# Kernel optimization log

Hardware: AMD Instinct MI355X
Metric: run time of the kernel (lower is better)

## Reference

```python
import jax, jax.numpy as jnp
import numpy as np

NUM_AGES = 100
FEAT_DIM = 512
BATCH = 4096
TEMPERATURE = 0.1
EPS = 1e-6


def setup_inputs() -> dict:
    key = jax.random.key(0)
    k1, k2, k3 = jax.random.split(key, 3)
    z_age = jax.random.normal(k1, (BATCH, FEAT_DIM), dtype=jnp.float32)
    ages = jax.random.randint(k2, (BATCH,), 0, NUM_AGES, dtype=jnp.int64)
    proxies = jax.random.normal(k3, (NUM_AGES, FEAT_DIM), dtype=jnp.float32)
    return {"z_age": z_age, "ages": ages, "proxies": proxies}


def _unit_diff(a, b):
    d = a - b
    return d / (jnp.linalg.norm(d, axis=-1, keepdims=True) + EPS)


def reference(z_age, ages, proxies):
    # Vectorized equivalent of the O(B^2) python double loop.
    # Only pairs with age_i < age_j contribute (age_i > age_j branch is a no-op `...`).
    B = z_age.shape[0]
    A = proxies.shape[0]
    aj = ages.astype(jnp.int32)
    c_cur = proxies[aj]                                   # [B, D]
    c_next = proxies[jnp.minimum(aj + 1, A - 1)]          # [B, D]
    c_prev = proxies[jnp.maximum(aj - 1, 0)]              # [B, D]
    vf = _unit_diff(c_next, c_cur)                        # forward direction per sample j
    vb = _unit_diff(c_prev, c_cur)                        # backward direction per sample j

    # Pairwise norms via Gram matrix: ||z_i - z_j||.
    G = z_age @ z_age.T                                   # [B, B]
    sq = jnp.diagonal(G)                                  # [B]
    d2 = jnp.maximum(sq[:, None] + sq[None, :] - 2.0 * G, 0.0)
    norm = jnp.sqrt(d2)                                   # [B, B]
    denom = norm + EPS

    # dot(v_d_ij, v_f_j) = (z_i . vf_j - z_j . vf_j) / (||z_i - z_j|| + eps)
    Gf = z_age @ vf.T                                     # [B, B], Gf[i, j] = z_i . vf_j
    Gb = z_age @ vb.T
    dot_f = (Gf - jnp.diagonal(Gf)[None, :]) / denom
    dot_b = (Gb - jnp.diagonal(Gb)[None, :]) / denom

    # -log(exp(df/T) / (exp(df/T) + exp(db/T))) = softplus((db - df)/T)
    per_pair = jax.nn.softplus((dot_b - dot_f) / TEMPERATURE)  # [B, B]
    mask = ages[:, None] < ages[None, :]
    loss = jnp.sum(jnp.where(mask, per_pair, 0.0))
    return loss / (B * (B - 1))
```

## Files before the change

kernel.cpp:

```cpp
#include <hip/hip_runtime.h>
#include <hip/hip_bf16.h>

#define NUM_AGES 100
#define FEAT 512
#define BATCH 4096
#define EPSF 1e-6f
#define INV_T 10.0f
#define INV_NORM (1.0f / ((float)BATCH * (float)(BATCH - 1)))

#define BM 128
#define BN 64
#define BK 64
#define NTILES 1056
#define NXCD 8
#define CHUNK (NTILES / NXCD)

typedef __bf16 bf16_t;
typedef __bf16 v8bf __attribute__((ext_vector_type(8)));
typedef float v4f __attribute__((ext_vector_type(4)));

__device__ __forceinline__ void async16(const void* g, void* l) {
  __builtin_amdgcn_global_load_lds(
      (const __attribute__((address_space(1))) void*)g,
      (__attribute__((address_space(3))) void*)l, 16, 0, 0);
}

__global__ __launch_bounds__(256) void prep_kernel(
    const float* __restrict__ z, const int* __restrict__ ages,
    const float* __restrict__ proxies,
    bf16_t* __restrict__ zb, bf16_t* __restrict__ wb,
    float* __restrict__ sq, float* __restrict__ hd,
    int* __restrict__ ages_s, float* __restrict__ out)
{
  int j = blockIdx.x;
  int t = threadIdx.x;
  if (j == 0 && t == 0) out[0] = 0.0f;

  int araw = ages[j];
  int a = araw < 0 ? 0 : (araw > NUM_AGES - 1 ? NUM_AGES - 1 : araw);
  const float* cc = proxies + (size_t)a * FEAT;
  const float* cn = proxies + (size_t)(a + 1 > NUM_AGES - 1 ? NUM_AGES - 1 : a + 1) * FEAT;
  const float* cp = proxies + (size_t)(a - 1 < 0 ? 0 : a - 1) * FEAT;
  const float* zr = z + (size_t)j * FEAT;

  int cnt = 0;
#pragma unroll
  for (int e = 0; e < BATCH / 256; ++e) {
    int k = t + e * 256;
    int ak = ages[k];
    cnt += (ak < araw || (ak == araw && k < j)) ? 1 : 0;
  }

  int c0 = 2 * t;
  float2 cc2 = *(const float2*)(cc + c0);
  float2 cn2 = *(const float2*)(cn + c0);
  float2 cp2 = *(const float2*)(cp + c0);
  float2 z2  = *(const float2*)(zr + c0);
  float df0 = cn2.x - cc2.x, df1 = cn2.y - cc2.y;
  float db0 = cp2.x - cc2.x, db1 = cp2.y - cc2.y;
  float s_ff = df0 * df0 + df1 * df1;
  float s_bb = db0 * db0 + db1 * db1;
  float s_zz = z2.x * z2.x + z2.y * z2.y;
  float s_zf = z2.x * df0 + z2.y * df1;
  float s_zb = z2.x * db0 + z2.y * db1;

  float fcnt = (float)cnt;
#pragma unroll
  for (int off = 32; off > 0; off >>= 1) {
    s_ff += __shfl_down(s_ff, off, 64);
    s_bb += __shfl_down(s_bb, off, 64);
    s_zz += __shfl_down(s_zz, off, 64);
    s_zf += __shfl_down(s_zf, off, 64);
    s_zb += __shfl_down(s_zb, off, 64);
    fcnt += __shfl_down(fcnt, off, 64);
  }
  __shared__ float red[4][6];
  int wv = t >> 6, lane = t & 63;
  if (lane == 0) {
    red[wv][0] = s_ff; red[wv][1] = s_bb; red[wv][2] = s_zz;
    red[wv][3] = s_zf; red[wv][4] = s_zb; red[wv][5] = fcnt;
  }
  __syncthreads();
  float ff = red[0][0] + red[1][0] + red[2][0] + red[3][0];
  float bb = red[0][1] + red[1][1] + red[2][1] + red[3][1];
  float zz = red[0][2] + red[1][2] + red[2][2] + red[3][2];
  float zdf = red[0][3] + red[1][3] + red[2][3] + red[3][3];
  float zdb = red[0][4] + red[1][4] + red[2][4] + red[3][4];
  int rank = (int)(red[0][5] + red[1][5] + red[2][5] + red[3][5]);

  float rf = 1.0f / (sqrtf(ff) + EPSF);
  float rb = 1.0f / (sqrtf(bb) + EPSF);
  int key = rank & 7;
  int c2s = (c0 & ~63) | (((((c0 >> 3) & 7) ^ key) << 3)) | (c0 & 7);
  float w0 = db0 * rb - df0 * rf;
  float w1 = db1 * rb - df1 * rf;
  union { bf16_t h[2]; unsigned u; } uz, uw;
  uz.h[0] = (bf16_t)z2.x; uz.h[1] = (bf16_t)z2.y;
  uw.h[0] = (bf16_t)w0;   uw.h[1] = (bf16_t)w1;
  *(unsigned*)((char*)zb + ((size_t)rank * FEAT + c2s) * 2) = uz.u;
  *(unsigned*)((char*)wb + ((size_t)rank * FEAT + c2s) * 2) = uw.u;
  if (t == 0) {
    sq[rank] = zz;
    hd[rank] = rb * zdb - rf * zdf;
    ages_s[rank] = araw;
  }
}

__global__ __launch_bounds__(256, 2) void pair_kernel(
    const bf16_t* __restrict__ zb, const bf16_t* __restrict__ wb,
    const float* __restrict__ sq, const float* __restrict__ hd,
    const int* __restrict__ ages, float* __restrict__ out)
{
  __shared__ __attribute__((aligned(16))) char lds[2][32768];
  __shared__ float s_sqi[BM];
  __shared__ int   s_agei[BM];
  __shared__ float s_sqj[BN];
  __shared__ float s_hdj[BN];
  __shared__ int   s_agej[BN];
  __shared__ float wsum[4];

  int t = threadIdx.x;
  int wv = t >> 6, lane = t & 63;

  int by = 0, bx = 0;
  {
    int rem = (blockIdx.x & 7) * CHUNK + (blockIdx.x >> 3);
    int done = 0;
    for (int sy = 0; sy < 4 && !done; ++sy) {
      for (int sx = 0; sx < 8 && !done; ++sx) {
        int cnt = 0;
        for (int r = 0; r < 8; ++r) {
          int b = 8 * sy + r;
          int lo = 2 * b; if (lo < 8 * sx) lo = 8 * sx;
          int ww = 8 * sx + 8 - lo; if (ww < 0) ww = 0;
          cnt += ww;
        }
        if (rem < cnt) {
          for (int r = 0; r < 8 && !done; ++r) {
            int b = 8 * sy + r;
            int lo = 2 * b; if (lo < 8 * sx) lo = 8 * sx;
            int ww = 8 * sx + 8 - lo; if (ww < 0) ww = 0;
            if (rem < ww) { by = b; bx = lo + rem; done = 1; }
            else rem -= ww;
          }
        } else {
          rem -= cnt;
        }
      }
    }
  }
  int i0 = by * BM, j0 = bx * BN;

  if (t < BM) {
    s_sqi[t] = sq[i0 + t];
    s_agei[t] = ages[i0 + t];
  } else if (t < BM + BN) {
    int u = t - BM;
    s_sqj[u] = sq[j0 + u];
    s_hdj[u] = hd[j0 + u];
    s_agej[u] = ages[j0 + u];
  }

  v4f accG[4][2], accH[4][2];
#pragma unroll
  for (int a = 0; a < 4; ++a)
#pragma unroll
    for (int b = 0; b < 2; ++b) {
      accG[a][b] = (v4f){0.f, 0.f, 0.f, 0.f};
      accH[a][b] = (v4f){0.f, 0.f, 0.f, 0.f};
    }

  int wm = wv >> 1, wn = wv & 1;
  int lm = lane & 15, q = lane >> 4;
  int psw0 = ((q     ) ^ (lm & 7)) * 16;
  int psw1 = ((q + 4 ) ^ (lm & 7)) * 16;

  int loff = (lane >> 3) * FEAT + (lane & 7) * 8;
  const bf16_t* baseA = zb + (size_t)i0 * FEAT + loff;
  const bf16_t* baseZ = zb + (size_t)j0 * FEAT + loff;
  const bf16_t* baseW = wb + (size_t)j0 * FEAT + loff;

#pragma unroll
  for (int c = 0; c < 4; ++c) {
    int chunk = wv * 4 + c;
    async16(baseA + (size_t)chunk * 8 * FEAT, lds[0] + chunk * 1024);
  }
#pragma unroll
  for (int c = 0; c < 2; ++c) {
    int chunk = wv * 2 + c;
    async16(baseZ + (size_t)chunk * 8 * FEAT, lds[0] + 16384 + chunk * 1024);
    async16(baseW + (size_t)chunk * 8 * FEAT, lds[0] + 24576 + chunk * 1024);
  }
  __syncthreads();

  int cur = 0;
  for (int it = 0; it < FEAT / BK; ++it) {
    if (it + 1 < FEAT / BK) {
      int k0n = (it + 1) * BK;
      char* nb = lds[cur ^ 1];
#pragma unroll
      for (int c = 0; c < 4; ++c) {
        int chunk = wv * 4 + c;
        async16(baseA + (size_t)chunk * 8 * FEAT + k0n, nb + chunk * 1024);
      }
#pragma unroll
      for (int c = 0; c < 2; ++c) {
        int chunk = wv * 2 + c;
        async16(baseZ + (size_t)chunk * 8 * FEAT + k0n, nb + 16384 + chunk * 1024);
        async16(baseW + (size_t)chunk * 8 * FEAT + k0n, nb + 24576 + chunk * 1024);
      }
    }

    const char* cb = lds[cur];
#pragma unroll
    for (int s = 0; s < 2; ++s) {
      int psw = s ? psw1 : psw0;
      v8bf afr[4], bz[2], bw[2];
#pragma unroll
      for (int mi = 0; mi < 4; ++mi) {
        int r = wm * 64 + mi * 16 + lm;
        afr[mi] = *(const v8bf*)(cb + r * 128 + psw);
      }
#pragma unroll
      for (int ni = 0; ni < 2; ++ni) {
        int r = wn * 32 + ni * 16 + lm;
        bz[ni] = *(const v8bf*)(cb + 16384 + r * 128 + psw);
        bw[ni] = *(const v8bf*)(cb + 24576 + r * 128 + psw);
      }
#pragma unroll
      for (int mi = 0; mi < 4; ++mi)
#pragma unroll
        for (int ni = 0; ni < 2; ++ni) {
          accG[mi][ni] = __builtin_amdgcn_mfma_f32_16x16x32_bf16(afr[mi], bz[ni], accG[mi][ni], 0, 0, 0);
          accH[mi][ni] = __builtin_amdgcn_mfma_f32_16x16x32_bf16(afr[mi], bw[ni], accH[mi][ni], 0, 0, 0);
        }
    }

    if (it + 1 < FEAT / BK) {
      __syncthreads();
      cur ^= 1;
    }
  }

  float tsum = 0.f;
#pragma unroll
  for (int ni = 0; ni < 2; ++ni) {
    int jl = wn * 32 + ni * 16 + lm;
    float sqj = s_sqj[jl];
    float hdj = s_hdj[jl];
    int aj = s_agej[jl];
#pragma unroll
    for (int mi = 0; mi < 4; ++mi) {
#pragma unroll
      for (int r = 0; r < 4; ++r) {
        int il = wm * 64 + mi * 16 + q * 4 + r;
        float g = accG[mi][ni][r];
        float h = accH[mi][ni][r];
        float d2 = fmaxf(s_sqi[il] + sqj - 2.0f * g, 1e-12f);
        float rs = __builtin_amdgcn_rsqf(d2);
        float arg = (h - hdj) * INV_T * rs;
        float sp = fmaxf(arg, 0.0f) + __logf(1.0f + __expf(-fabsf(arg)));
        tsum += (s_agei[il] < aj) ? sp : 0.0f;
      }
    }
  }

#pragma unroll
  for (int off = 32; off > 0; off >>= 1) tsum += __shfl_down(tsum, off, 64);
  if (lane == 0) wsum[wv] = tsum;
  __syncthreads();
  if (t == 0)
    atomicAdd(out, (wsum[0] + wsum[1] + wsum[2] + wsum[3]) * INV_NORM);
}

extern "C" void kernel_launch(void* const* d_in, const int* in_sizes, int n_in,
                              void* d_out, int out_size, void* d_ws, size_t ws_size,
                              hipStream_t stream) {
  const float* z = (const float*)d_in[0];
  const int* ages = (const int*)d_in[1];
  const float* proxies = (const float*)d_in[2];
  float* out = (float*)d_out;

  char* ws = (char*)d_ws;
  bf16_t* zb = (bf16_t*)ws;
  bf16_t* wb = (bf16_t*)(ws + (size_t)4 * 1024 * 1024);
  size_t o = (size_t)8 * 1024 * 1024;
  float* sq      = (float*)(ws + o);
  float* hd      = (float*)(ws + o + 16384);
  int*   ages_s  = (int*)  (ws + o + 32768);

  prep_kernel<<<BATCH, 256, 0, stream>>>(z, ages, proxies, zb, wb, sq, hd, ages_s, out);
  pair_kernel<<<NTILES, 256, 0, stream>>>(zb, wb, sq, hd, ages_s, out);
}
```

Before: 112.1 us.

## Prefetch two K-stages ahead with fine-grained vmcnt waits and MFMA priority

Restructures the double-buffered K loop so two stages are in flight at once. The next-next stage is issued after a barrier, and only the current stage's loads are waited on with an explicit vmcnt(8) rather than a full __syncthreads drain. MFMA blocks are wrapped in s_setprio to favour matrix issue, and sched_barriers pin the instruction order. The aim is to hide global-to-LDS latency behind compute, at the cost of hand-maintained waitcnt counts that become fragile if the number of loads per stage changes.

```diff
diff --git a/kernel.cpp b/kernel.cpp
--- a/kernel.cpp
+++ b/kernel.cpp
@@ -180,38 +180,31 @@
   const bf16_t* baseZ = zb + (size_t)j0 * FEAT + loff;
   const bf16_t* baseW = wb + (size_t)j0 * FEAT + loff;
 
-#pragma unroll
-  for (int c = 0; c < 4; ++c) {
-    int chunk = wv * 4 + c;
-    async16(baseA + (size_t)chunk * 8 * FEAT, lds[0] + chunk * 1024);
-  }
-#pragma unroll
-  for (int c = 0; c < 2; ++c) {
-    int chunk = wv * 2 + c;
-    async16(baseZ + (size_t)chunk * 8 * FEAT, lds[0] + 16384 + chunk * 1024);
-    async16(baseW + (size_t)chunk * 8 * FEAT, lds[0] + 24576 + chunk * 1024);
-  }
-  __syncthreads();
+  auto STAGE = [&](int k0, char* nb) {
+#pragma unroll
+    for (int c = 0; c < 4; ++c) {
+      int chunk = wv * 4 + c;
+      async16(baseA + (size_t)chunk * 8 * FEAT + k0, nb + chunk * 1024);
+    }
+#pragma unroll
+    for (int c = 0; c < 2; ++c) {
+      int chunk = wv * 2 + c;
+      async16(baseZ + (size_t)chunk * 8 * FEAT + k0, nb + 16384 + chunk * 1024);
+      async16(baseW + (size_t)chunk * 8 * FEAT + k0, nb + 24576 + chunk * 1024);
+    }
+  };
+
+  STAGE(0, lds[0]);
+  __builtin_amdgcn_sched_barrier(0);
+  STAGE(BK, lds[1]);
+  __builtin_amdgcn_sched_barrier(0);
+  asm volatile("s_waitcnt vmcnt(8) lgkmcnt(0)" ::: "memory");
+  __builtin_amdgcn_s_barrier();
+  __builtin_amdgcn_sched_barrier(0);
 
   int cur = 0;
   for (int it = 0; it < FEAT / BK; ++it) {
-    if (it + 1 < FEAT / BK) {
-      int k0n = (it + 1) * BK;
-      char* nb = lds[cur ^ 1];
-#pragma unroll
-      for (int c = 0; c < 4; ++c) {
-        int chunk = wv * 4 + c;
-        async16(baseA + (size_t)chunk * 8 * FEAT + k0n, nb + chunk * 1024);
-      }
-#pragma unroll
-      for (int c = 0; c < 2; ++c) {
-        int chunk = wv * 2 + c;
-        async16(baseZ + (size_t)chunk * 8 * FEAT + k0n, nb + 16384 + chunk * 1024);
-        async16(baseW + (size_t)chunk * 8 * FEAT + k0n, nb + 24576 + chunk * 1024);
-      }
-    }
-
-    const char* cb = lds[cur];
+    const char* cb = lds[cur & 1];
 #pragma unroll
     for (int s = 0; s < 2; ++s) {
       int psw = s ? psw1 : psw0;
@@ -227,6 +220,7 @@
         bz[ni] = *(const v8bf*)(cb + 16384 + r * 128 + psw);
         bw[ni] = *(const v8bf*)(cb + 24576 + r * 128 + psw);
       }
+      __builtin_amdgcn_s_setprio(1);
 #pragma unroll
       for (int mi = 0; mi < 4; ++mi)
 #pragma unroll
@@ -234,12 +228,23 @@
           accG[mi][ni] = __builtin_amdgcn_mfma_f32_16x16x32_bf16(afr[mi], bz[ni], accG[mi][ni], 0, 0, 0);
           accH[mi][ni] = __builtin_amdgcn_mfma_f32_16x16x32_bf16(afr[mi], bw[ni], accH[mi][ni], 0, 0, 0);
         }
-    }
-
-    if (it + 1 < FEAT / BK) {
-      __syncthreads();
-      cur ^= 1;
-    }
+      __builtin_amdgcn_s_setprio(0);
+    }
+    __builtin_amdgcn_sched_barrier(0);
+
+    if (it + 2 < FEAT / BK) {
+      __builtin_amdgcn_s_barrier();
+      __builtin_amdgcn_sched_barrier(0);
+      STAGE((it + 2) * BK, lds[cur & 1]);
+      __builtin_amdgcn_sched_barrier(0);
+      asm volatile("s_waitcnt vmcnt(8)" ::: "memory");
+      __builtin_amdgcn_s_barrier();
+    } else if (it + 1 < FEAT / BK) {
+      asm volatile("s_waitcnt vmcnt(0)" ::: "memory");
+      __builtin_amdgcn_s_barrier();
+    }
+    __builtin_amdgcn_sched_barrier(0);
+    cur ^= 1;
   }
 
   float tsum = 0.f;
```

Measured after the change: 112.8 us. Within noise of the previous version (+0.6%).
